# Kernel tuning notes

Hardware: AMD Instinct MI355X
Metric: run time of the kernel (lower is better)

Reference implementation:

```python
import jax, jax.numpy as jnp
import numpy as np

EMBED_DIM = 1024
NUM_HEADS = 16
DIM_HEAD = EMBED_DIM // NUM_HEADS


def setup_inputs() -> dict:
    key = jax.random.key(0)
    ks = jax.random.split(key, 9)
    s = 1.0 / np.sqrt(EMBED_DIM)
    x = jax.random.normal(ks[0], (2, 2048, EMBED_DIM), dtype=jnp.float32)
    Wq = jax.random.uniform(ks[1], (EMBED_DIM, EMBED_DIM), jnp.float32, -s, s)
    bq = jax.random.uniform(ks[2], (EMBED_DIM,), jnp.float32, -s, s)
    Wk = jax.random.uniform(ks[3], (EMBED_DIM, EMBED_DIM), jnp.float32, -s, s)
    bk = jax.random.uniform(ks[4], (EMBED_DIM,), jnp.float32, -s, s)
    Wv = jax.random.uniform(ks[5], (EMBED_DIM, EMBED_DIM), jnp.float32, -s, s)
    bv = jax.random.uniform(ks[6], (EMBED_DIM,), jnp.float32, -s, s)
    Wo = jax.random.uniform(ks[7], (EMBED_DIM, EMBED_DIM), jnp.float32, -s, s)
    bo = jax.random.uniform(ks[8], (EMBED_DIM,), jnp.float32, -s, s)
    return {"x": x, "Wq": Wq, "bq": bq, "Wk": Wk, "bk": bk,
            "Wv": Wv, "bv": bv, "Wo": Wo, "bo": bo}


def reference(x, Wq, bq, Wk, bk, Wv, bv, Wo, bo):
    B, S, _ = x.shape
    # Linear layers (torch nn.Linear: x @ W.T + b), reshape to heads
    Q = (x @ Wq.T + bq).reshape(B, S, NUM_HEADS, DIM_HEAD)
    K = (x @ Wk.T + bk).reshape(B, S, NUM_HEADS, DIM_HEAD)
    V = (x @ Wv.T + bv).reshape(B, S, NUM_HEADS, DIM_HEAD)
    scores = jnp.einsum('bqhd,bkhd->bhqk', Q, K) / np.sqrt(DIM_HEAD)
    attn = jax.nn.softmax(scores, axis=-1)
    context = jnp.einsum('bhqk,bkhd->bqhd', attn, V).reshape(B, S, EMBED_DIM)
    return context @ Wo.T + bo
```

## Files before the change

### kernel.cpp

```cpp
#include <hip/hip_runtime.h>
#include <hip/hip_bf16.h>

#define SEQ   2048
#define EMB   1024
#define NHEAD 16
#define DHEAD 64
#define BATCH 2
#define MTOT  (BATCH*SEQ)
#define QT    128
#define KT    64

typedef __attribute__((ext_vector_type(8))) short s8v;
typedef __attribute__((ext_vector_type(4))) short s4v;
typedef __attribute__((ext_vector_type(4))) float f4v;

__device__ __forceinline__ float b2f(short s) {
    union { unsigned u; float f; } v;
    v.u = ((unsigned)(unsigned short)s) << 16;
    return v.f;
}
__device__ __forceinline__ short f2b(float f) {
    union { float fl; unsigned u; } v; v.fl = f;
    unsigned u = v.u;
    u = (u + 0x7fffu + ((u >> 16) & 1u)) >> 16;
    return (short)u;
}
__device__ __forceinline__ unsigned pk2(float a, float b) {
    union { __hip_bfloat162 h; unsigned u; } c;
    c.h = __float22bfloat162_rn(float2{a, b});
    return c.u;
}
__device__ __forceinline__ float b2f_lo(unsigned u) {
    union { unsigned x; float f; } v; v.x = u << 16; return v.f;
}
__device__ __forceinline__ float b2f_hi(unsigned u) {
    union { unsigned x; float f; } v; v.x = u & 0xffff0000u; return v.f;
}

__device__ __forceinline__ void bar_lds() {
    asm volatile("s_waitcnt lgkmcnt(0)\n\ts_barrier" ::: "memory");
}

__global__ __launch_bounds__(256)
void cvt_bf16(const float* __restrict__ s0, const float* __restrict__ s1,
              const float* __restrict__ s2, const float* __restrict__ s3,
              const float* __restrict__ s4,
              short* __restrict__ d0, short* __restrict__ d1,
              short* __restrict__ d2, short* __restrict__ d3,
              short* __restrict__ d4)
{
    const int seg = blockIdx.y;
    const float* s = seg == 0 ? s0 : seg == 1 ? s1 : seg == 2 ? s2 : seg == 3 ? s3 : s4;
    short*       d = seg == 0 ? d0 : seg == 1 ? d1 : seg == 2 ? d2 : seg == 3 ? d3 : d4;
    const int n4 = (seg == 0 ? MTOT * EMB : EMB * EMB) / 4;
    const int stride = gridDim.x * 256;
    for (int i = blockIdx.x * 256 + threadIdx.x; i < n4; i += stride) {
        const float4 v = ((const float4*)s)[i];
        s4v o;
        o[0] = f2b(v.x); o[1] = f2b(v.y); o[2] = f2b(v.z); o[3] = f2b(v.w);
        ((s4v*)d)[i] = o;
    }
}

template<int NT, bool FUSED3>
__global__ __launch_bounds__(256, 3)
void gemm_bb2(const short* __restrict__ A,
              const short* __restrict__ W0, const short* __restrict__ W1, const short* __restrict__ W2,
              const float* __restrict__ B0, const float* __restrict__ B1, const float* __restrict__ B2,
              void* __restrict__ C0, void* __restrict__ C1, void* __restrict__ C2)
{
    constexpr int JN = NT / 32;
    constexpr int WP = NT / 32;
    const int K = EMB, N = EMB;
    const int ntiles = EMB / NT;
    const int mat = blockIdx.x / ntiles;
    const int n0  = (blockIdx.x % ntiles) * NT;
    const int m0  = blockIdx.y * 128;
    const short* W  = (mat == 0) ? W0 : (mat == 1 ? W1 : W2);
    const float* Bi = (mat == 0) ? B0 : (mat == 1 ? B1 : B2);
    void*        C  = (mat == 0) ? C0 : (mat == 1 ? C1 : C2);

    __shared__ __align__(16) short As[128 * 72];
    __shared__ __align__(16) short Ws[NT * 72];

    const int tid  = threadIdx.x;
    const int lane = tid & 63;
    const int wave = tid >> 6;
    const int quad = lane >> 4;
    const int l16  = lane & 15;
    const int wm   = wave >> 1;
    const int wn   = wave & 1;

    f4v acc[4][JN] = {};

    const int c = tid & 7;
    const int r = tid >> 3;

    s8v ra[4], rw[WP];
    #pragma unroll
    for (int p = 0; p < 4; ++p)
        ra[p] = *(const s8v*)(A + (size_t)(m0 + r + p * 32) * K + c * 8);
    #pragma unroll
    for (int p = 0; p < WP; ++p)
        rw[p] = *(const s8v*)(W + (size_t)(n0 + r + p * 32) * K + c * 8);

    for (int k0 = 0; k0 < K; k0 += 64) {
        if (k0) bar_lds();
        #pragma unroll
        for (int p = 0; p < 4; ++p)
            *(s8v*)(As + (r + p * 32) * 72 + c * 8) = ra[p];
        #pragma unroll
        for (int p = 0; p < WP; ++p)
            *(s8v*)(Ws + (r + p * 32) * 72 + c * 8) = rw[p];
        if (k0 + 64 < K) {
            #pragma unroll
            for (int p = 0; p < 4; ++p)
                ra[p] = *(const s8v*)(A + (size_t)(m0 + r + p * 32) * K + k0 + 64 + c * 8);
            #pragma unroll
            for (int p = 0; p < WP; ++p)
                rw[p] = *(const s8v*)(W + (size_t)(n0 + r + p * 32) * K + k0 + 64 + c * 8);
        }
        bar_lds();

        #pragma unroll
        for (int kk = 0; kk < 2; ++kk) {
            const int ko = kk * 32 + quad * 8;
            s8v af[4], wf[JN];
            #pragma unroll
            for (int i = 0; i < 4; ++i)
                af[i] = *(const s8v*)(As + (wm * 64 + i * 16 + l16) * 72 + ko);
            #pragma unroll
            for (int j = 0; j < JN; ++j)
                wf[j] = *(const s8v*)(Ws + (wn * (NT / 2) + j * 16 + l16) * 72 + ko);
            #pragma unroll
            for (int i = 0; i < 4; ++i)
                #pragma unroll
                for (int j = 0; j < JN; ++j)
                    acc[i][j] = __builtin_amdgcn_mfma_f32_16x16x32_bf16(
                        af[i], wf[j], acc[i][j], 0, 0, 0);
        }
    }

    #pragma unroll
    for (int j = 0; j < JN; ++j) {
        const int n = n0 + wn * (NT / 2) + j * 16 + l16;
        const float bv = Bi[n];
        #pragma unroll
        for (int i = 0; i < 4; ++i) {
            const int mb = m0 + wm * 64 + i * 16 + quad * 4;
            if (FUSED3 && mat == 2) {
                const int bb = mb >> 11, s = mb & 2047;
                s4v ov;
                #pragma unroll
                for (int rr = 0; rr < 4; ++rr) ov[rr] = f2b(acc[i][j][rr] + bv);
                *(s4v*)((short*)C + ((size_t)(bb * 1024 + n)) * SEQ + s) = ov;
            } else if (FUSED3) {
                #pragma unroll
                for (int rr = 0; rr < 4; ++rr)
                    ((short*)C)[(size_t)(mb + rr) * N + n] = f2b(acc[i][j][rr] + bv);
            } else {
                #pragma unroll
                for (int rr = 0; rr < 4; ++rr)
                    ((float*)C)[(size_t)(mb + rr) * N + n] = acc[i][j][rr] + bv;
            }
        }
    }
}

__global__ __launch_bounds__(256, 2)
void attn_mfma4(const short* Q, const short* __restrict__ Kg,
                const short* __restrict__ Vt, short* O)
{
    const int blk = blockIdx.x;
    const int qb = blk & 15;
    const int h  = (blk >> 4) & 15;
    const int b  = blk >> 8;
    const int q0 = qb * QT;

    const int tid  = threadIdx.x;
    const int lane = tid & 63;
    const int wave = tid >> 6;
    const int quad = lane >> 4;
    const int l16  = lane & 15;

    __shared__ __align__(16) short Ks[2][64 * 72];
    __shared__ __align__(16) short Vs[2][64 * 72];
    __shared__ __align__(16) short Pt[QT * 72];

    s8v qf[2][2];
    #pragma unroll
    for (int mi = 0; mi < 2; ++mi)
        #pragma unroll
        for (int kk = 0; kk < 2; ++kk)
            qf[mi][kk] = *(const s8v*)(Q + (size_t)(b * SEQ + q0 + wave * 32 + mi * 16 + l16) * EMB
                                         + h * DHEAD + kk * 32 + quad * 8);

    f4v   oacc[4][2] = {};
    float lsum[2] = {};

    const int c = tid & 7, r = tid >> 3;
    const size_t kbase = (size_t)(b * SEQ) * EMB + h * DHEAD;
    const size_t vbase = (size_t)((b * NHEAD + h) * DHEAD) * SEQ;

    s8v ka[2], va[2];
    #pragma unroll
    for (int p = 0; p < 2; ++p) {
        ka[p] = *(const s8v*)(Kg + kbase + (size_t)(r + p * 32) * EMB + c * 8);
        va[p] = *(const s8v*)(Vt + vbase + (size_t)(r + p * 32) * SEQ + c * 8);
    }

    for (int t = 0; t < SEQ / KT; ++t) {
        const int buf = t & 1;
        short* KsB = Ks[buf];
        short* VsB = Vs[buf];

        #pragma unroll
        for (int p = 0; p < 2; ++p) {
            *(s8v*)(KsB + (r + p * 32) * 72 + c * 8) = ka[p];
            *(s8v*)(VsB + (r + p * 32) * 72 + c * 8) = va[p];
        }
        if (t + 1 < SEQ / KT) {
            const int kt2 = (t + 1) * KT;
            #pragma unroll
            for (int p = 0; p < 2; ++p) {
                ka[p] = *(const s8v*)(Kg + kbase + (size_t)(kt2 + r + p * 32) * EMB + c * 8);
                va[p] = *(const s8v*)(Vt + vbase + (size_t)(r + p * 32) * SEQ + kt2 + c * 8);
            }
        }
        bar_lds();

        f4v sc[4][2] = {};
        #pragma unroll
        for (int kk = 0; kk < 2; ++kk) {
            const int ko = kk * 32 + quad * 8;
            s8v kf[4];
            #pragma unroll
            for (int j = 0; j < 4; ++j)
                kf[j] = *(const s8v*)(KsB + (j * 16 + l16) * 72 + ko);
            #pragma unroll
            for (int j = 0; j < 4; ++j)
                #pragma unroll
                for (int mi = 0; mi < 2; ++mi)
                    sc[j][mi] = __builtin_amdgcn_mfma_f32_16x16x32_bf16(
                        kf[j], qf[mi][kk], sc[j][mi], 0, 0, 0);
        }

        #pragma unroll
        for (int j = 0; j < 4; ++j)
            #pragma unroll
            for (int mi = 0; mi < 2; ++mi) {
                const float p0 = __expf(sc[j][mi][0] * 0.125f);
                const float p1 = __expf(sc[j][mi][1] * 0.125f);
                const float p2 = __expf(sc[j][mi][2] * 0.125f);
                const float p3 = __expf(sc[j][mi][3] * 0.125f);
                union { unsigned u[2]; s4v s; } pv;
                pv.u[0] = pk2(p0, p1);
                pv.u[1] = pk2(p2, p3);
                lsum[mi] += (b2f_lo(pv.u[0]) + b2f_hi(pv.u[0]))
                          + (b2f_lo(pv.u[1]) + b2f_hi(pv.u[1]));
                *(s4v*)(Pt + (wave * 32 + mi * 16 + l16) * 72 + j * 16 + quad * 4) = pv.s;
            }

        #pragma unroll
        for (int kk = 0; kk < 2; ++kk) {
            const int ko = kk * 32 + quad * 8;
            s8v pf[2];
            #pragma unroll
            for (int mi = 0; mi < 2; ++mi)
                pf[mi] = *(const s8v*)(Pt + (wave * 32 + mi * 16 + l16) * 72 + ko);
            #pragma unroll
            for (int j = 0; j < 4; ++j) {
                const s8v vf = *(const s8v*)(VsB + (j * 16 + l16) * 72 + ko);
                #pragma unroll
                for (int mi = 0; mi < 2; ++mi)
                    oacc[j][mi] = __builtin_amdgcn_mfma_f32_16x16x32_bf16(
                        vf, pf[mi], oacc[j][mi], 0, 0, 0);
            }
        }
    }

    #pragma unroll
    for (int mi = 0; mi < 2; ++mi) {
        float s = lsum[mi];
        s += __shfl_xor(s, 16);
        s += __shfl_xor(s, 32);
        lsum[mi] = 1.0f / s;
    }

    #pragma unroll
    for (int j = 0; j < 4; ++j)
        #pragma unroll
        for (int mi = 0; mi < 2; ++mi) {
            union { unsigned u[2]; s4v s; } ov;
            ov.u[0] = pk2(oacc[j][mi][0] * lsum[mi], oacc[j][mi][1] * lsum[mi]);
            ov.u[1] = pk2(oacc[j][mi][2] * lsum[mi], oacc[j][mi][3] * lsum[mi]);
            *(s4v*)(Pt + (wave * 32 + mi * 16 + l16) * 72 + j * 16 + quad * 4) = ov.s;
        }

    const int row = tid >> 1;
    const int off = (tid & 1) * 32;
    #pragma unroll
    for (int c4 = 0; c4 < 4; ++c4) {
        const s8v t = *(const s8v*)(Pt + row * 72 + off + c4 * 8);
        *(s8v*)(O + (size_t)(b * SEQ + q0 + row) * EMB + h * DHEAD + off + c4 * 8) = t;
    }
}

extern "C" void kernel_launch(void* const* d_in, const int* in_sizes, int n_in,
                              void* d_out, int out_size, void* d_ws, size_t ws_size,
                              hipStream_t stream)
{
    const float* x  = (const float*)d_in[0];
    const float* Wq = (const float*)d_in[1];
    const float* bq = (const float*)d_in[2];
    const float* Wk = (const float*)d_in[3];
    const float* bk = (const float*)d_in[4];
    const float* Wv = (const float*)d_in[5];
    const float* bv = (const float*)d_in[6];
    const float* Wo = (const float*)d_in[7];
    const float* bo = (const float*)d_in[8];
    float* out = (float*)d_out;

    short* xb  = (short*)d_ws;
    short* Wqb = xb  + (size_t)MTOT * EMB;
    short* Wkb = Wqb + (size_t)EMB * EMB;
    short* Wvb = Wkb + (size_t)EMB * EMB;
    short* Wob = Wvb + (size_t)EMB * EMB;
    short* Qw  = Wob + (size_t)EMB * EMB;
    short* Kw  = Qw  + (size_t)MTOT * EMB;
    short* Vtw = Kw  + (size_t)MTOT * EMB;

    cvt_bf16<<<dim3(1024, 5), 256, 0, stream>>>(x, Wq, Wk, Wv, Wo,
                                                xb, Wqb, Wkb, Wvb, Wob);

    gemm_bb2<128, true><<<dim3(24, 32), 256, 0, stream>>>(
        xb, Wqb, Wkb, Wvb, bq, bk, bv, Qw, Kw, Vtw);

    attn_mfma4<<<dim3(BATCH * NHEAD * (SEQ / QT)), 256, 0, stream>>>(Qw, Kw, Vtw, Qw);

    gemm_bb2<64, false><<<dim3(16, 32), 256, 0, stream>>>(
        Qw, Wob, Wob, Wob, bo, bo, bo, out, out, out);
}
```

Measured before the change: 199.6 us.

## Load GEMM tiles directly to LDS with XOR-swizzled layout

The GEMM kernels now stage A and W tiles through direct global-to-LDS loads instead of register staging plus LDS stores. To avoid bank conflicts without padding, the conversion kernel and the attention output writer store bf16 data with an XOR swizzle of the 16-byte chunks within each row, and the GEMM fragment reads undo it. The register double-buffer prefetch is removed, so each k-step now loads, syncs and computes with two barriers, which may expose load latency.

Measured after the change: 194.7 us. 1.03x faster.

```diff
diff --git a/kernel.cpp b/kernel.cpp
--- a/kernel.cpp
+++ b/kernel.cpp
@@ -41,36 +41,46 @@
     asm volatile("s_waitcnt lgkmcnt(0)\n\ts_barrier" ::: "memory");
 }
 
+__device__ __forceinline__ void gl_lds16(const short* g, short* l) {
+    __builtin_amdgcn_global_load_lds(
+        (const __attribute__((address_space(1))) void*)g,
+        (__attribute__((address_space(3))) void*)l, 16, 0, 0);
+}
+
 __global__ __launch_bounds__(256)
-void cvt_bf16(const float* __restrict__ s0, const float* __restrict__ s1,
-              const float* __restrict__ s2, const float* __restrict__ s3,
-              const float* __restrict__ s4,
-              short* __restrict__ d0, short* __restrict__ d1,
-              short* __restrict__ d2, short* __restrict__ d3,
-              short* __restrict__ d4)
+void cvt_swz(const float* __restrict__ s0, const float* __restrict__ s1,
+             const float* __restrict__ s2, const float* __restrict__ s3,
+             const float* __restrict__ s4,
+             short* __restrict__ d0, short* __restrict__ d1,
+             short* __restrict__ d2, short* __restrict__ d3,
+             short* __restrict__ d4)
 {
     const int seg = blockIdx.y;
     const float* s = seg == 0 ? s0 : seg == 1 ? s1 : seg == 2 ? s2 : seg == 3 ? s3 : s4;
     short*       d = seg == 0 ? d0 : seg == 1 ? d1 : seg == 2 ? d2 : seg == 3 ? d3 : d4;
-    const int n4 = (seg == 0 ? MTOT * EMB : EMB * EMB) / 4;
+    const int nchunk = (seg == 0 ? MTOT * EMB : EMB * EMB) / 8;
     const int stride = gridDim.x * 256;
-    for (int i = blockIdx.x * 256 + threadIdx.x; i < n4; i += stride) {
-        const float4 v = ((const float4*)s)[i];
-        s4v o;
-        o[0] = f2b(v.x); o[1] = f2b(v.y); o[2] = f2b(v.z); o[3] = f2b(v.w);
-        ((s4v*)d)[i] = o;
+    for (int i = blockIdx.x * 256 + threadIdx.x; i < nchunk; i += stride) {
+        const int row = i >> 7;
+        const int c   = i & 127;
+        const float4 v0 = *(const float4*)(s + (size_t)i * 8);
+        const float4 v1 = *(const float4*)(s + (size_t)i * 8 + 4);
+        s8v o;
+        o[0] = f2b(v0.x); o[1] = f2b(v0.y); o[2] = f2b(v0.z); o[3] = f2b(v0.w);
+        o[4] = f2b(v1.x); o[5] = f2b(v1.y); o[6] = f2b(v1.z); o[7] = f2b(v1.w);
+        const int cp = (c & ~7) | ((c & 7) ^ (row & 7));
+        *(s8v*)(d + (size_t)row * EMB + cp * 8) = o;
     }
 }
 
 template<int NT, bool FUSED3>
 __global__ __launch_bounds__(256, 3)
-void gemm_bb2(const short* __restrict__ A,
+void gemm_bb3(const short* __restrict__ A,
               const short* __restrict__ W0, const short* __restrict__ W1, const short* __restrict__ W2,
               const float* __restrict__ B0, const float* __restrict__ B1, const float* __restrict__ B2,
               void* __restrict__ C0, void* __restrict__ C1, void* __restrict__ C2)
 {
     constexpr int JN = NT / 32;
-    constexpr int WP = NT / 32;
     const int K = EMB, N = EMB;
     const int ntiles = EMB / NT;
     const int mat = blockIdx.x / ntiles;
@@ -80,58 +90,48 @@
     const float* Bi = (mat == 0) ? B0 : (mat == 1 ? B1 : B2);
     void*        C  = (mat == 0) ? C0 : (mat == 1 ? C1 : C2);
 
-    __shared__ __align__(16) short As[128 * 72];
-    __shared__ __align__(16) short Ws[NT * 72];
+    __shared__ __align__(16) short As[128 * 64];
+    __shared__ __align__(16) short Ws[NT * 64];
 
     const int tid  = threadIdx.x;
     const int lane = tid & 63;
     const int wave = tid >> 6;
     const int quad = lane >> 4;
     const int l16  = lane & 15;
+    const int l8   = l16 & 7;
     const int wm   = wave >> 1;
     const int wn   = wave & 1;
 
     f4v acc[4][JN] = {};
 
-    const int c = tid & 7;
-    const int r = tid >> 3;
-
-    s8v ra[4], rw[WP];
-    #pragma unroll
-    for (int p = 0; p < 4; ++p)
-        ra[p] = *(const s8v*)(A + (size_t)(m0 + r + p * 32) * K + c * 8);
-    #pragma unroll
-    for (int p = 0; p < WP; ++p)
-        rw[p] = *(const s8v*)(W + (size_t)(n0 + r + p * 32) * K + c * 8);
+    const int srow = lane >> 3;
+    const int scol = (lane & 7) * 8;
 
     for (int k0 = 0; k0 < K; k0 += 64) {
-        if (k0) bar_lds();
-        #pragma unroll
-        for (int p = 0; p < 4; ++p)
-            *(s8v*)(As + (r + p * 32) * 72 + c * 8) = ra[p];
-        #pragma unroll
-        for (int p = 0; p < WP; ++p)
-            *(s8v*)(Ws + (r + p * 32) * 72 + c * 8) = rw[p];
-        if (k0 + 64 < K) {
-            #pragma unroll
-            for (int p = 0; p < 4; ++p)
-                ra[p] = *(const s8v*)(A + (size_t)(m0 + r + p * 32) * K + k0 + 64 + c * 8);
-            #pragma unroll
-            for (int p = 0; p < WP; ++p)
-                rw[p] = *(const s8v*)(W + (size_t)(n0 + r + p * 32) * K + k0 + 64 + c * 8);
-        }
-        bar_lds();
+        #pragma unroll
+        for (int p = 0; p < 4; ++p) {
+            const int rbase = wave * 32 + p * 8;
+            gl_lds16(A + (size_t)(m0 + rbase + srow) * K + k0 + scol,
+                     As + rbase * 64);
+        }
+        #pragma unroll
+        for (int p = 0; p < NT / 32; ++p) {
+            const int rbase = wave * (NT / 4) + p * 8;
+            gl_lds16(W + (size_t)(n0 + rbase + srow) * K + k0 + scol,
+                     Ws + rbase * 64);
+        }
+        __syncthreads();
 
         #pragma unroll
         for (int kk = 0; kk < 2; ++kk) {
-            const int ko = kk * 32 + quad * 8;
+            const int slot = ((kk * 4 + quad) ^ l8) * 8;
             s8v af[4], wf[JN];
             #pragma unroll
             for (int i = 0; i < 4; ++i)
-                af[i] = *(const s8v*)(As + (wm * 64 + i * 16 + l16) * 72 + ko);
+                af[i] = *(const s8v*)(As + (wm * 64 + i * 16 + l16) * 64 + slot);
             #pragma unroll
             for (int j = 0; j < JN; ++j)
-                wf[j] = *(const s8v*)(Ws + (wn * (NT / 2) + j * 16 + l16) * 72 + ko);
+                wf[j] = *(const s8v*)(Ws + (wn * (NT / 2) + j * 16 + l16) * 64 + slot);
             #pragma unroll
             for (int i = 0; i < 4; ++i)
                 #pragma unroll
@@ -139,6 +139,7 @@
                     acc[i][j] = __builtin_amdgcn_mfma_f32_16x16x32_bf16(
                         af[i], wf[j], acc[i][j], 0, 0, 0);
         }
+        __syncthreads();
     }
 
     #pragma unroll
@@ -298,11 +299,13 @@
         }
 
     const int row = tid >> 1;
-    const int off = (tid & 1) * 32;
+    const int cb  = (tid & 1) * 4;
     #pragma unroll
     for (int c4 = 0; c4 < 4; ++c4) {
-        const s8v t = *(const s8v*)(Pt + row * 72 + off + c4 * 8);
-        *(s8v*)(O + (size_t)(b * SEQ + q0 + row) * EMB + h * DHEAD + off + c4 * 8) = t;
+        const int lc = cb + c4;
+        const s8v t = *(const s8v*)(Pt + row * 72 + lc * 8);
+        *(s8v*)(O + (size_t)(b * SEQ + q0 + row) * EMB + h * DHEAD
+                  + ((lc ^ (row & 7)) * 8)) = t;
     }
 }
 
@@ -330,14 +333,14 @@
     short* Kw  = Qw  + (size_t)MTOT * EMB;
     short* Vtw = Kw  + (size_t)MTOT * EMB;
 
-    cvt_bf16<<<dim3(1024, 5), 256, 0, stream>>>(x, Wq, Wk, Wv, Wo,
-                                                xb, Wqb, Wkb, Wvb, Wob);
-
-    gemm_bb2<128, true><<<dim3(24, 32), 256, 0, stream>>>(
+    cvt_swz<<<dim3(512, 5), 256, 0, stream>>>(x, Wq, Wk, Wv, Wo,
+                                              xb, Wqb, Wkb, Wvb, Wob);
+
+    gemm_bb3<128, true><<<dim3(24, 32), 256, 0, stream>>>(
         xb, Wqb, Wkb, Wvb, bq, bk, bv, Qw, Kw, Vtw);
 
     attn_mfma4<<<dim3(BATCH * NHEAD * (SEQ / QT)), 256, 0, stream>>>(Qw, Kw, Vtw, Qw);
 
-    gemm_bb2<64, false><<<dim3(16, 32), 256, 0, stream>>>(
+    gemm_bb3<64, false><<<dim3(16, 32), 256, 0, stream>>>(
         Qw, Wob, Wob, Wob, bo, bo, bo, out, out, out);
 }
```
